# Kernel optimization log

Hardware: AMD Instinct MI355X
Metric: run time of the kernel (lower is better)

The kernel has to match this reference:

```python
import jax, jax.numpy as jnp
import numpy as np

B, T, N_EMBD, HEAD = 4, 4096, 1024, 64


def setup_inputs() -> dict:
    key = jax.random.key(0)
    k1, k2, k3, k4 = jax.random.split(key, 4)
    x = jax.random.normal(k1, (B, T, N_EMBD), dtype=jnp.float32)
    # nn.Linear weights, stored as [in, out] so y = x @ W
    s = 1.0 / np.sqrt(N_EMBD)
    Wq = jax.random.uniform(k2, (N_EMBD, HEAD), dtype=jnp.float32, minval=-s, maxval=s)
    Wk = jax.random.uniform(k3, (N_EMBD, HEAD), dtype=jnp.float32, minval=-s, maxval=s)
    Wv = jax.random.uniform(k4, (N_EMBD, HEAD), dtype=jnp.float32, minval=-s, maxval=s)
    return {"x": x, "Wq": Wq, "Wk": Wk, "Wv": Wv}


def reference(x, Wq, Wk, Wv):
    # x: [B, T, C] with C = n_embd; note: original scales by sqrt(C), not sqrt(head_size)
    T_, C = x.shape[1], x.shape[2]
    q = x @ Wq            # [B, T, H]
    k = x @ Wk            # [B, T, H]
    v = x @ Wv            # [B, T, H]
    scale = 1.0 / jnp.sqrt(jnp.asarray(C, dtype=x.dtype))
    w = jnp.einsum('bqh,bkh->bqk', q, k) * scale  # [B, T, T]
    causal = jnp.tril(jnp.ones((T_, T_), dtype=bool))
    w = jnp.where(causal, w, -jnp.inf)
    attn = jax.nn.softmax(w, axis=-1)
    # dropout in eval mode (identity) for deterministic reference
    return attn @ v       # [B, T, H]
```

## Files before the change

kernel.cpp:

```cpp
#include <hip/hip_runtime.h>

constexpr int B_  = 4;
constexpr int T_  = 4096;
constexpr int C_  = 1024;
constexpr int H_  = 64;
constexpr int BT_ = B_ * T_;
constexpr int NUNIT_ = 1152;

typedef __attribute__((ext_vector_type(4))) float f32x4;
typedef __attribute__((ext_vector_type(8))) short bf16x8;
typedef __attribute__((ext_vector_type(8))) unsigned short u16x8;
typedef __attribute__((ext_vector_type(4))) unsigned short u16x4;

__device__ __forceinline__ unsigned short f32_to_bf16(float f) {
    union { float f; unsigned int u; } v;
    v.f = f;
    unsigned int r = v.u + 0x7FFFu + ((v.u >> 16) & 1u);
    return (unsigned short)(r >> 16);
}
__device__ __forceinline__ float bf16_to_f32(unsigned short us) {
    union { unsigned int u; float f; } v;
    v.u = (unsigned int)us << 16;
    return v.f;
}
__device__ __forceinline__ float exp2_hw(float x) {
    return __builtin_amdgcn_exp2f(x);
}

__global__ __launch_bounds__(256) void wconv_kernel(
    const float* __restrict__ Wq, const float* __restrict__ Wk,
    const float* __restrict__ Wv, unsigned short* __restrict__ Wt)
{
    const int tid  = threadIdx.x;
    const int wid  = blockIdx.x * 4 + (tid >> 6);
    const int lane = tid & 63;
    const int q    = lane >> 4, c = lane & 15;
    const int ntile = wid >> 5;
    const int kstep = wid & 31;
    const int n = ntile * 16 + c;
    const int m = n >> 6;
    const float* W = (m == 0) ? Wq : (m == 1) ? Wk : Wv;
    const int ncol = n & 63;
    const int k0 = kstep * 32 + q * 8;
    u16x8 pk;
#pragma unroll
    for (int j = 0; j < 8; j++) pk[j] = f32_to_bf16(W[(size_t)(k0 + j) * H_ + ncol]);
    *(u16x8*)(Wt + (size_t)wid * 512 + lane * 8) = pk;
}

__global__ __launch_bounds__(512, 4) void proj_kernel(
    const float* __restrict__ x, const unsigned short* __restrict__ Wt,
    unsigned short* __restrict__ Qf, unsigned short* __restrict__ Kf,
    unsigned short* __restrict__ Vf)
{
    __shared__ __align__(16) unsigned short xs[32][72];
    const int t    = threadIdx.x;
    const int r0   = blockIdx.x * 32;
    const int w    = t >> 6;
    const int lane = t & 63;
    const int quad = lane >> 4;
    const int c    = lane & 15;
    const int mh   = (w >> 2) * 16;
    const int nh   = (w & 3) * 48;
    const int srow = t >> 4;
    const int koff = (t & 15) * 4;

    f32x4 acc[3];
#pragma unroll
    for (int j = 0; j < 3; j++) acc[j] = {0.f, 0.f, 0.f, 0.f};

    const float* xp = x + (size_t)(r0 + srow) * C_ + koff;
    f32x4 v0 = *(const f32x4*)xp;

    for (int kk = 0; kk < C_; kk += 64) {
        u16x4 p;
#pragma unroll
        for (int i = 0; i < 4; i++) p[i] = f32_to_bf16(v0[i]);
        __syncthreads();
        *(u16x4*)&xs[srow][koff] = p;
        __syncthreads();
        if (kk + 64 < C_) v0 = *(const f32x4*)(xp + kk + 64);
#pragma unroll
        for (int ks = 0; ks < 64; ks += 32) {
            const bf16x8 a0 = *(const bf16x8*)&xs[mh + c][ks + quad * 8];
            const unsigned short* bp =
                Wt + ((size_t)(nh >> 4) * 32 + ((kk + ks) >> 5)) * 512 + lane * 8;
#pragma unroll
            for (int j = 0; j < 3; j++) {
                const bf16x8 bj = *(const bf16x8*)(bp + (size_t)j * 32 * 512);
                acc[j] = __builtin_amdgcn_mfma_f32_16x16x32_bf16(a0, bj, acc[j], 0, 0, 0);
            }
        }
    }

    const int S   = r0 + mh;
    const int bS  = S >> 12;
    const int cc0 = quad * 4;
#pragma unroll
    for (int j = 0; j < 3; j++) {
        const int nt = nh + j * 16;
        if (nt < 128) {
            const int d0 = (nt < 64) ? nt : nt - 64;
            unsigned short* base = (nt < 64) ? Qf : Kf;
            const int t16  = (S & 4095) >> 4;
            const int half = d0 >> 5;
            const int q8   = ((d0 >> 4) & 1) * 2 + (c >> 3);
            const int j8   = c & 7;
            unsigned short* p = base + ((size_t)(bS * 256 + t16)) * 1024
                              + half * 512 + q8 * 128 + j8;
#pragma unroll
            for (int r = 0; r < 4; r++) p[(cc0 + r) * 8] = f32_to_bf16(acc[j][r]);
        } else {
            const int d0  = nt - 128;
            const int k32 = (S & 4095) >> 5;
            const int ht  = d0 >> 4;
            const int sq  = (S & 31) >> 3;
            unsigned short* p = Vf + (((size_t)(bS * 128 + k32)) * 4 + ht) * 512 + c * 8;
#pragma unroll
            for (int r = 0; r < 4; r++) {
                const int cc = cc0 + r;
                p[(sq + (cc >> 3)) * 128 + (cc & 7)] = f32_to_bf16(acc[j][r]);
            }
        }
    }
}

__global__ __launch_bounds__(256) void attn_kernel(
    const unsigned short* __restrict__ Qf, const unsigned short* __restrict__ Kf,
    const unsigned short* __restrict__ Vf, unsigned short* __restrict__ Opg,
    float* __restrict__ mlg)
{
    __shared__ __align__(16) unsigned short Pb[4][16][72];
    const int tid  = threadIdx.x;
    const int w    = tid >> 6;
    const int lane = tid & 63;
    const int quad = lane >> 4;
    const int c    = lane & 15;
    const int bid  = blockIdx.x;
    const int qt   = 255 - (bid & 255);
    const int ks   = bid >> 8;
    const int g    = qt >> 5;
    if (ks > g) return;
    const int b    = w;
    const int q0   = qt * 16;
    const int k0   = ks * 512;
    const int kend = (q0 + 15 < k0 + 511) ? q0 + 15 : k0 + 511;

    const unsigned short* qp = Qf + ((size_t)b * 256 + qt) * 1024 + lane * 8;
    const bf16x8 qB0 = *(const bf16x8*)qp;
    const bf16x8 qB1 = *(const bf16x8*)(qp + 512);

    f32x4 O[4];
#pragma unroll
    for (int tt = 0; tt < 4; tt++) O[tt] = {0.f, 0.f, 0.f, 0.f};
    float m = -1e30f, ls = 0.f;
    const float scale2 = 0.045084436f;

    unsigned short* P = &Pb[w][0][0];
    const int prow = c * 72;

    for (int kb = k0; kb <= kend; kb += 64) {
        const unsigned short* kfb = Kf + ((size_t)b * 256 + (kb >> 4)) * 1024 + lane * 8;
        f32x4 S[4];
#pragma unroll
        for (int tt = 0; tt < 4; tt++) {
            const bf16x8 kA0 = *(const bf16x8*)(kfb + tt * 1024);
            const bf16x8 kA1 = *(const bf16x8*)(kfb + tt * 1024 + 512);
            f32x4 s = {0.f, 0.f, 0.f, 0.f};
            s = __builtin_amdgcn_mfma_f32_16x16x32_bf16(kA0, qB0, s, 0, 0, 0);
            s = __builtin_amdgcn_mfma_f32_16x16x32_bf16(kA1, qB1, s, 0, 0, 0);
            S[tt] = s;
        }
        float sc[16];
        if (kb + 63 > q0) {
#pragma unroll
            for (int tt = 0; tt < 4; tt++)
#pragma unroll
                for (int r = 0; r < 4; r++) {
                    const int key = kb + tt * 16 + quad * 4 + r;
                    sc[tt * 4 + r] = (key > q0 + c) ? -1e30f : S[tt][r] * scale2;
                }
        } else {
#pragma unroll
            for (int tt = 0; tt < 4; tt++)
#pragma unroll
                for (int r = 0; r < 4; r++) sc[tt * 4 + r] = S[tt][r] * scale2;
        }
        float mx = sc[0];
#pragma unroll
        for (int i = 1; i < 16; i++) mx = fmaxf(mx, sc[i]);
        mx = fmaxf(mx, __shfl_xor(mx, 16));
        mx = fmaxf(mx, __shfl_xor(mx, 32));
        const float mn    = fmaxf(m, mx);
        const float alpha = exp2_hw(m - mn);
        m = mn;
        float lsum = 0.f;
#pragma unroll
        for (int tt = 0; tt < 4; tt++) {
            u16x4 pk;
#pragma unroll
            for (int r = 0; r < 4; r++) {
                const float e = exp2_hw(sc[tt * 4 + r] - mn);
                lsum += e;
                pk[r] = f32_to_bf16(e);
            }
            *(u16x4*)(P + prow + tt * 16 + quad * 4) = pk;
        }
        ls = ls * alpha + lsum;
#pragma unroll
        for (int tt = 0; tt < 4; tt++)
#pragma unroll
            for (int r = 0; r < 4; r++) O[tt][r] *= alpha;

        const bf16x8 pB0 = *(const bf16x8*)(P + prow + quad * 8);
        const bf16x8 pB1 = *(const bf16x8*)(P + prow + 32 + quad * 8);

        const unsigned short* vfb = Vf + ((size_t)b * 128 + (kb >> 5)) * 2048 + lane * 8;
#pragma unroll
        for (int tt = 0; tt < 4; tt++) {
            const bf16x8 vA0 = *(const bf16x8*)(vfb + tt * 512);
            const bf16x8 vA1 = *(const bf16x8*)(vfb + 2048 + tt * 512);
            O[tt] = __builtin_amdgcn_mfma_f32_16x16x32_bf16(vA0, pB0, O[tt], 0, 0, 0);
            O[tt] = __builtin_amdgcn_mfma_f32_16x16x32_bf16(vA1, pB1, O[tt], 0, 0, 0);
        }
    }

    ls += __shfl_xor(ls, 16);
    ls += __shfl_xor(ls, 32);

    const size_t ustore = (size_t)b * NUNIT_ + qt + 16 * g * (g - 1) + g * (qt & 31) + ks;
#pragma unroll
    for (int tt = 0; tt < 4; tt++) {
        u16x4 pk;
#pragma unroll
        for (int r = 0; r < 4; r++) pk[r] = f32_to_bf16(O[tt][r]);
        *(u16x4*)(Opg + ustore * 1024 + c * 64 + tt * 16 + quad * 4) = pk;
    }
    if (lane < 16) {
        mlg[ustore * 32 + c]      = m;
        mlg[ustore * 32 + 16 + c] = ls;
    }
}

__global__ __launch_bounds__(256) void merge_kernel(
    const unsigned short* __restrict__ Opg, const float* __restrict__ mlg,
    float* __restrict__ out)
{
    const int idx = blockIdx.x;
    const int b   = idx >> 8;
    const int qt  = idx & 255;
    const int g   = qt >> 5;
    const int nseg = g + 1;
    const size_t base = (size_t)b * NUNIT_ + qt + 16 * g * (g - 1) + g * (qt & 31);
    const int t  = threadIdx.x;
    const int h  = t & 63;
    const int rg = t >> 6;
#pragma unroll
    for (int i = 0; i < 4; i++) {
        const int row = rg * 4 + i;
        float M = -1e30f;
        for (int s = 0; s < nseg; s++) M = fmaxf(M, mlg[(base + s) * 32 + row]);
        float L = 0.f, val = 0.f;
        for (int s = 0; s < nseg; s++) {
            const float e = exp2_hw(mlg[(base + s) * 32 + row] - M);
            L   = fmaf(mlg[(base + s) * 32 + 16 + row], e, L);
            val = fmaf(bf16_to_f32(Opg[(base + s) * 1024 + row * 64 + h]), e, val);
        }
        out[((size_t)b * T_ + qt * 16 + row) * H_ + h] = val / L;
    }
}

extern "C" void kernel_launch(void* const* d_in, const int* in_sizes, int n_in,
                              void* d_out, int out_size, void* d_ws, size_t ws_size,
                              hipStream_t stream) {
    const float* x  = (const float*)d_in[0];
    const float* Wq = (const float*)d_in[1];
    const float* Wk = (const float*)d_in[2];
    const float* Wv = (const float*)d_in[3];
    float* out = (float*)d_out;

    unsigned short* Qf = (unsigned short*)d_ws;
    unsigned short* Kf = Qf + (size_t)BT_ * H_;
    unsigned short* Vf = Kf + (size_t)BT_ * H_;
    unsigned short* Wt = Vf + (size_t)BT_ * H_;
    unsigned short* Opg = Wt + (size_t)192 * C_;
    float*          mlg = (float*)(Opg + (size_t)B_ * NUNIT_ * 1024);

    wconv_kernel<<<96, 256, 0, stream>>>(Wq, Wk, Wv, Wt);
    proj_kernel<<<BT_ / 32, 512, 0, stream>>>(x, Wt, Qf, Kf, Vf);
    attn_kernel<<<2048, 256, 0, stream>>>(Qf, Kf, Vf, Opg, mlg);
    merge_kernel<<<1024, 256, 0, stream>>>(Opg, mlg, out);
}
```

Before: 167.8 us.

## Retile projection into 16-row half-width blocks with double-buffered LDS

The projection kernel changes from 512-thread blocks covering 32 rows and all 192 outputs to 128-thread blocks covering 16 rows and half of the outputs, launched as 2048 blocks. The LDS staging buffer for x is double-buffered, which cuts the barriers in the K loop from two to one. The aim is more, smaller blocks and less barrier stalling. The cost is that each row of x is now read and converted twice, once per output half, which raises global memory traffic unless the cache absorbs it.

New measurement: 170.4 us. No clear change (+1.5%).

```diff
diff --git a/kernel.cpp b/kernel.cpp
--- a/kernel.cpp
+++ b/kernel.cpp
@@ -48,41 +48,50 @@
     *(u16x8*)(Wt + (size_t)wid * 512 + lane * 8) = pk;
 }
 
-__global__ __launch_bounds__(512, 4) void proj_kernel(
+__global__ __launch_bounds__(128, 4) void proj_kernel(
     const float* __restrict__ x, const unsigned short* __restrict__ Wt,
     unsigned short* __restrict__ Qf, unsigned short* __restrict__ Kf,
     unsigned short* __restrict__ Vf)
 {
-    __shared__ __align__(16) unsigned short xs[32][72];
-    const int t    = threadIdx.x;
-    const int r0   = blockIdx.x * 32;
-    const int w    = t >> 6;
-    const int lane = t & 63;
-    const int quad = lane >> 4;
-    const int c    = lane & 15;
-    const int mh   = (w >> 2) * 16;
-    const int nh   = (w & 3) * 48;
-    const int srow = t >> 4;
-    const int koff = (t & 15) * 4;
+    __shared__ __align__(16) unsigned short xs[2][16][72];
+    const int t     = threadIdx.x;
+    const int mtile = blockIdx.x & 1023;
+    const int half_ = blockIdx.x >> 10;
+    const int r0    = mtile * 16;
+    const int w     = t >> 6;
+    const int lane  = t & 63;
+    const int quad  = lane >> 4;
+    const int c     = lane & 15;
+    const int nh    = half_ * 96 + w * 48;
+    const int row   = t >> 3;
+    const int koff  = (t & 7) * 4;
 
     f32x4 acc[3];
 #pragma unroll
     for (int j = 0; j < 3; j++) acc[j] = {0.f, 0.f, 0.f, 0.f};
 
-    const float* xp = x + (size_t)(r0 + srow) * C_ + koff;
+    const float* xp = x + (size_t)(r0 + row) * C_ + koff;
     f32x4 v0 = *(const f32x4*)xp;
-
+    f32x4 v1 = *(const f32x4*)(xp + 32);
+
+    int p = 0;
     for (int kk = 0; kk < C_; kk += 64) {
-        u16x4 p;
-#pragma unroll
-        for (int i = 0; i < 4; i++) p[i] = f32_to_bf16(v0[i]);
+        u16x4 pk0, pk1;
+#pragma unroll
+        for (int i = 0; i < 4; i++) {
+            pk0[i] = f32_to_bf16(v0[i]);
+            pk1[i] = f32_to_bf16(v1[i]);
+        }
+        *(u16x4*)&xs[p][row][koff]      = pk0;
+        *(u16x4*)&xs[p][row][koff + 32] = pk1;
         __syncthreads();
-        *(u16x4*)&xs[srow][koff] = p;
-        __syncthreads();
-        if (kk + 64 < C_) v0 = *(const f32x4*)(xp + kk + 64);
+        if (kk + 64 < C_) {
+            v0 = *(const f32x4*)(xp + kk + 64);
+            v1 = *(const f32x4*)(xp + kk + 96);
+        }
 #pragma unroll
         for (int ks = 0; ks < 64; ks += 32) {
-            const bf16x8 a0 = *(const bf16x8*)&xs[mh + c][ks + quad * 8];
+            const bf16x8 a0 = *(const bf16x8*)&xs[p][c][ks + quad * 8];
             const unsigned short* bp =
                 Wt + ((size_t)(nh >> 4) * 32 + ((kk + ks) >> 5)) * 512 + lane * 8;
 #pragma unroll
@@ -91,9 +100,10 @@
                 acc[j] = __builtin_amdgcn_mfma_f32_16x16x32_bf16(a0, bj, acc[j], 0, 0, 0);
             }
         }
-    }
-
-    const int S   = r0 + mh;
+        p ^= 1;
+    }
+
+    const int S   = r0;
     const int bS  = S >> 12;
     const int cc0 = quad * 4;
 #pragma unroll
@@ -106,20 +116,20 @@
             const int half = d0 >> 5;
             const int q8   = ((d0 >> 4) & 1) * 2 + (c >> 3);
             const int j8   = c & 7;
-            unsigned short* p = base + ((size_t)(bS * 256 + t16)) * 1024
-                              + half * 512 + q8 * 128 + j8;
-#pragma unroll
-            for (int r = 0; r < 4; r++) p[(cc0 + r) * 8] = f32_to_bf16(acc[j][r]);
+            unsigned short* pq = base + ((size_t)(bS * 256 + t16)) * 1024
+                               + half * 512 + q8 * 128 + j8;
+#pragma unroll
+            for (int r = 0; r < 4; r++) pq[(cc0 + r) * 8] = f32_to_bf16(acc[j][r]);
         } else {
             const int d0  = nt - 128;
             const int k32 = (S & 4095) >> 5;
             const int ht  = d0 >> 4;
             const int sq  = (S & 31) >> 3;
-            unsigned short* p = Vf + (((size_t)(bS * 128 + k32)) * 4 + ht) * 512 + c * 8;
+            unsigned short* pv = Vf + (((size_t)(bS * 128 + k32)) * 4 + ht) * 512 + c * 8;
 #pragma unroll
             for (int r = 0; r < 4; r++) {
                 const int cc = cc0 + r;
-                p[(sq + (cc >> 3)) * 128 + (cc & 7)] = f32_to_bf16(acc[j][r]);
+                pv[(sq + (cc >> 3)) * 128 + (cc & 7)] = f32_to_bf16(acc[j][r]);
             }
         }
     }
@@ -287,7 +297,7 @@
     float*          mlg = (float*)(Opg + (size_t)B_ * NUNIT_ * 1024);
 
     wconv_kernel<<<96, 256, 0, stream>>>(Wq, Wk, Wv, Wt);
-    proj_kernel<<<BT_ / 32, 512, 0, stream>>>(x, Wt, Qf, Kf, Vf);
+    proj_kernel<<<2048, 128, 0, stream>>>(x, Wt, Qf, Kf, Vf);
     attn_kernel<<<2048, 256, 0, stream>>>(Qf, Kf, Vf, Opg, mlg);
     merge_kernel<<<1024, 256, 0, stream>>>(Opg, mlg, out);
 }
```
